# Optimization experiments

Measured on AMD Instinct MI355X. Metric: run time of the kernel, lower is better.

## Reference

```python
import jax, jax.numpy as jnp
import numpy as np
import math

SIZE = 112
GROUPS = 64

def _dct_filter(size):
    # get_dct_filter: W[i, j] = a_i * cos(pi * i / size * (j + 0.5)), a_0 = sqrt(1/size), else sqrt(2/size)
    i = np.arange(size)[:, None].astype(np.float64)
    j = np.arange(size)[None, :].astype(np.float64)
    a = np.where(i == 0, math.sqrt(1.0 / size), math.sqrt(2.0 / size))
    return (a * np.cos(np.pi * i / size * (j + 0.5))).astype(np.float32)

def _band_mask(size, groups):
    # Faithful to the source: d = sqrt((xx ^ 2) + (yy ^ 2)) where ^ is PYTHON BITWISE XOR (a bug in the
    # original, reproduced here). Keep entry if i*mul <= d < (i+1)*mul, else overwrite with 1e-8.
    mul = size // 8
    xs = np.bitwise_xor(np.arange(size), 2).astype(np.float64)
    d = np.sqrt(xs[:, None] + xs[None, :])            # [size, size], indexed [xx, yy]
    i = np.arange(groups).astype(np.float64)[:, None, None]
    keep = (d[None, :, :] >= i * mul) & (d[None, :, :] < (i + 1) * mul)  # [groups, size, size]
    return keep

_MASK = jnp.asarray(_band_mask(SIZE, GROUPS))

def setup_inputs() -> dict:
    key = jax.random.key(0)
    x = jax.random.normal(key, (64, GROUPS, SIZE, SIZE), dtype=jnp.float32)
    W = jnp.asarray(_dct_filter(SIZE))  # module's DCT-II basis buffer
    return {"x": x, "W": W}

def reference(x, W):
    # 2D DCT-II over spatial dims expressed as two matmuls with the module's own DCT filter:
    # Y[b,c] = W @ X[b,c] @ W^T   (fused replacement for the CPU round-trip dct(x))
    y = jnp.einsum('ik,bckl,jl->bcij', W, x, W)
    # Static radial-band mask per frequency group; outside-band entries are set to 1e-8.
    return jnp.where(_MASK[None], y, jnp.float32(1e-8))
```

## Files before the change

### kernel.cpp

```cpp
#include <hip/hip_runtime.h>


#define SIZE  112
#define TILE  (SIZE * SIZE)
#define TILE4 (TILE / 4)
#define NCOMPUTE 512
#define FILLV 1e-8f

#define DOT4(a, b) ((a).x*(b).x + (a).y*(b).y + (a).z*(b).z + (a).w*(b).w)

__global__ __launch_bounds__(256)
void dct_band_kernel(const float* __restrict__ x,
                     const float* __restrict__ W,
                     float* __restrict__ out)
{
    const int tid = threadIdx.x;
    const int blk = blockIdx.x;

    if (blk >= NCOMPUTE) {
        const int f = blk - NCOMPUTE;
        const int b = f / 62;
        const int c = 2 + f % 62;
        float4* o4 = (float4*)(out + (size_t)(b * 64 + c) * TILE);
        const float4 v = make_float4(FILLV, FILLV, FILLV, FILLV);
        #pragma unroll
        for (int n = 0; n < 13; ++n) {
            int e = tid + n * 256;
            if (e < TILE4) o4[e] = v;
        }
        return;
    }

    __shared__ float4 regA[3248];
    __shared__ float4 Usm[784];

    const int q  = blk & 3;
    const int t  = blk >> 2;
    const int b  = t >> 1;
    const int c  = t & 1;
    const int i0 = 28 * q;
    const size_t tOff = (size_t)(b * 64 + c) * TILE;

    const float4* x4 = (const float4*)(x + tOff);
    #pragma unroll
    for (int n = 0; n < 13; ++n) {
        int e = tid + n * 256;
        if (e < TILE4) regA[e] = x4[e];
    }
    __syncthreads();

    if (tid < 196) {
        const int diq = tid / 28;
        const int l4  = tid % 28;
        float4 u0 = make_float4(0,0,0,0), u1 = u0, u2 = u0, u3 = u0;
        const float* wr0 = W + (i0 + 4 * diq) * SIZE;
        const float* wr1 = wr0 + SIZE;
        const float* wr2 = wr1 + SIZE;
        const float* wr3 = wr2 + SIZE;
        #pragma unroll 4
        for (int k = 0; k < SIZE; ++k) {
            float4 xv = regA[k * 28 + l4];
            float w0 = wr0[k], w1 = wr1[k], w2 = wr2[k], w3 = wr3[k];
            u0.x += w0 * xv.x; u0.y += w0 * xv.y; u0.z += w0 * xv.z; u0.w += w0 * xv.w;
            u1.x += w1 * xv.x; u1.y += w1 * xv.y; u1.z += w1 * xv.z; u1.w += w1 * xv.w;
            u2.x += w2 * xv.x; u2.y += w2 * xv.y; u2.z += w2 * xv.z; u2.w += w2 * xv.w;
            u3.x += w3 * xv.x; u3.y += w3 * xv.y; u3.z += w3 * xv.z; u3.w += w3 * xv.w;
        }
        const int ub = 4 * diq * 28 + l4;
        Usm[ub]          = u0;
        Usm[ub + 28]     = u1;
        Usm[ub + 56]     = u2;
        Usm[ub + 84]     = u3;
    }
    __syncthreads();

    const float4* W4 = (const float4*)W;
    #pragma unroll
    for (int n = 0; n < 13; ++n) {
        int e = tid + n * 256;
        if (e < TILE4) {
            int j = e / 28;
            int p = e % 28;
            regA[(j >> 2) * 113 + (j & 3) * 28 + p] = W4[e];
        }
    }
    __syncthreads();

    if (tid < 196) {
        const int dq = tid / 28;
        const int jq = tid % 28;
        float acc[4][4];
        #pragma unroll
        for (int a = 0; a < 4; ++a)
            #pragma unroll
            for (int d = 0; d < 4; ++d) acc[a][d] = 0.f;

        const float4* Ur = Usm + 4 * dq * 28;
        const float4* Wb = regA + jq * 113;
        #pragma unroll 2
        for (int l = 0; l < 28; ++l) {
            float4 u0 = Ur[l], u1 = Ur[l + 28], u2 = Ur[l + 56], u3 = Ur[l + 84];
            float4 w0 = Wb[l], w1 = Wb[l + 28], w2 = Wb[l + 56], w3 = Wb[l + 84];
            acc[0][0] += DOT4(u0, w0); acc[0][1] += DOT4(u0, w1);
            acc[0][2] += DOT4(u0, w2); acc[0][3] += DOT4(u0, w3);
            acc[1][0] += DOT4(u1, w0); acc[1][1] += DOT4(u1, w1);
            acc[1][2] += DOT4(u1, w2); acc[1][3] += DOT4(u1, w3);
            acc[2][0] += DOT4(u2, w0); acc[2][1] += DOT4(u2, w1);
            acc[2][2] += DOT4(u2, w2); acc[2][3] += DOT4(u2, w3);
            acc[3][0] += DOT4(u3, w0); acc[3][1] += DOT4(u3, w1);
            acc[3][2] += DOT4(u3, w2); acc[3][3] += DOT4(u3, w3);
        }

        const int j0 = 4 * jq;
        const bool g1 = (c != 0);
        #pragma unroll
        for (int mi = 0; mi < 4; ++mi) {
            const int i  = i0 + 4 * dq + mi;
            const int xi = i ^ 2;
            float4 res;
            res.x = (((xi + ((j0 + 0) ^ 2)) < 196) != g1) ? acc[mi][0] : FILLV;
            res.y = (((xi + ((j0 + 1) ^ 2)) < 196) != g1) ? acc[mi][1] : FILLV;
            res.z = (((xi + ((j0 + 2) ^ 2)) < 196) != g1) ? acc[mi][2] : FILLV;
            res.w = (((xi + ((j0 + 3) ^ 2)) < 196) != g1) ? acc[mi][3] : FILLV;
            ((float4*)(out + tOff + (size_t)i * SIZE))[jq] = res;
        }
    }
}

extern "C" void kernel_launch(void* const* d_in, const int* in_sizes, int n_in,
                              void* d_out, int out_size, void* d_ws, size_t ws_size,
                              hipStream_t stream) {
    const float* x = (const float*)d_in[0];
    const float* W = (const float*)d_in[1];
    float* out = (float*)d_out;
    (void)in_sizes; (void)n_in; (void)out_size; (void)d_ws; (void)ws_size;
    dct_band_kernel<<<dim3(NCOMPUTE + 64 * 62), dim3(256), 0, stream>>>(x, W, out);
}
```

Baseline: 315.2 us.

## Stream x in k-chunks, read W from global, nontemporal fill stores

The first matmul now stages x in four 28-row chunks with a small shared buffer instead of loading the whole 112x112 tile, cutting shared memory from about 64KB to about 25KB so more blocks can be resident. The second stage reads W rows directly from global/L2 instead of staging a padded transposed copy in LDS. The fill-only blocks use nontemporal stores for the constant 1e-8 output. The trade-offs are extra barriers per chunk and uncached-in-LDS global W reads in the inner loop.

```diff
diff --git a/kernel.cpp b/kernel.cpp
--- a/kernel.cpp
+++ b/kernel.cpp
@@ -4,8 +4,11 @@
 #define SIZE  112
 #define TILE  (SIZE * SIZE)
 #define TILE4 (TILE / 4)
+#define ROW4  (SIZE / 4)
 #define NCOMPUTE 512
 #define FILLV 1e-8f
+
+typedef float floatx4 __attribute__((ext_vector_type(4)));
 
 #define DOT4(a, b) ((a).x*(b).x + (a).y*(b).y + (a).z*(b).z + (a).w*(b).w)
 
@@ -21,17 +24,17 @@
         const int f = blk - NCOMPUTE;
         const int b = f / 62;
         const int c = 2 + f % 62;
-        float4* o4 = (float4*)(out + (size_t)(b * 64 + c) * TILE);
-        const float4 v = make_float4(FILLV, FILLV, FILLV, FILLV);
+        floatx4* o4 = (floatx4*)(out + (size_t)(b * 64 + c) * TILE);
+        const floatx4 v = {FILLV, FILLV, FILLV, FILLV};
         #pragma unroll
         for (int n = 0; n < 13; ++n) {
             int e = tid + n * 256;
-            if (e < TILE4) o4[e] = v;
+            if (e < TILE4) __builtin_nontemporal_store(v, o4 + e);
         }
         return;
     }
 
-    __shared__ float4 regA[3248];
+    __shared__ float4 Xs[784];
     __shared__ float4 Usm[784];
 
     const int q  = blk & 3;
@@ -40,49 +43,44 @@
     const int c  = t & 1;
     const int i0 = 28 * q;
     const size_t tOff = (size_t)(b * 64 + c) * TILE;
+    const float4* x4 = (const float4*)(x + tOff);
 
-    const float4* x4 = (const float4*)(x + tOff);
-    #pragma unroll
-    for (int n = 0; n < 13; ++n) {
-        int e = tid + n * 256;
-        if (e < TILE4) regA[e] = x4[e];
+    const int diq = tid / 28;
+    const int l4  = tid % 28;
+    float4 u0 = make_float4(0,0,0,0), u1 = u0, u2 = u0, u3 = u0;
+
+    for (int kp = 0; kp < 4; ++kp) {
+        #pragma unroll
+        for (int n = 0; n < 4; ++n) {
+            int e = tid + n * 256;
+            if (e < 784) Xs[e] = x4[kp * 784 + e];
+        }
+        __syncthreads();
+
+        if (tid < 196) {
+            const float* wr0 = W + (i0 + 4 * diq) * SIZE + kp * 28;
+            const float* wr1 = wr0 + SIZE;
+            const float* wr2 = wr1 + SIZE;
+            const float* wr3 = wr2 + SIZE;
+            #pragma unroll 4
+            for (int k = 0; k < 28; ++k) {
+                float4 xv = Xs[k * 28 + l4];
+                float w0 = wr0[k], w1 = wr1[k], w2 = wr2[k], w3 = wr3[k];
+                u0.x += w0 * xv.x; u0.y += w0 * xv.y; u0.z += w0 * xv.z; u0.w += w0 * xv.w;
+                u1.x += w1 * xv.x; u1.y += w1 * xv.y; u1.z += w1 * xv.z; u1.w += w1 * xv.w;
+                u2.x += w2 * xv.x; u2.y += w2 * xv.y; u2.z += w2 * xv.z; u2.w += w2 * xv.w;
+                u3.x += w3 * xv.x; u3.y += w3 * xv.y; u3.z += w3 * xv.z; u3.w += w3 * xv.w;
+            }
+        }
+        __syncthreads();
     }
-    __syncthreads();
 
     if (tid < 196) {
-        const int diq = tid / 28;
-        const int l4  = tid % 28;
-        float4 u0 = make_float4(0,0,0,0), u1 = u0, u2 = u0, u3 = u0;
-        const float* wr0 = W + (i0 + 4 * diq) * SIZE;
-        const float* wr1 = wr0 + SIZE;
-        const float* wr2 = wr1 + SIZE;
-        const float* wr3 = wr2 + SIZE;
-        #pragma unroll 4
-        for (int k = 0; k < SIZE; ++k) {
-            float4 xv = regA[k * 28 + l4];
-            float w0 = wr0[k], w1 = wr1[k], w2 = wr2[k], w3 = wr3[k];
-            u0.x += w0 * xv.x; u0.y += w0 * xv.y; u0.z += w0 * xv.z; u0.w += w0 * xv.w;
-            u1.x += w1 * xv.x; u1.y += w1 * xv.y; u1.z += w1 * xv.z; u1.w += w1 * xv.w;
-            u2.x += w2 * xv.x; u2.y += w2 * xv.y; u2.z += w2 * xv.z; u2.w += w2 * xv.w;
-            u3.x += w3 * xv.x; u3.y += w3 * xv.y; u3.z += w3 * xv.z; u3.w += w3 * xv.w;
-        }
         const int ub = 4 * diq * 28 + l4;
-        Usm[ub]          = u0;
-        Usm[ub + 28]     = u1;
-        Usm[ub + 56]     = u2;
-        Usm[ub + 84]     = u3;
-    }
-    __syncthreads();
-
-    const float4* W4 = (const float4*)W;
-    #pragma unroll
-    for (int n = 0; n < 13; ++n) {
-        int e = tid + n * 256;
-        if (e < TILE4) {
-            int j = e / 28;
-            int p = e % 28;
-            regA[(j >> 2) * 113 + (j & 3) * 28 + p] = W4[e];
-        }
+        Usm[ub]      = u0;
+        Usm[ub + 28] = u1;
+        Usm[ub + 56] = u2;
+        Usm[ub + 84] = u3;
     }
     __syncthreads();
 
@@ -96,19 +94,23 @@
             for (int d = 0; d < 4; ++d) acc[a][d] = 0.f;
 
         const float4* Ur = Usm + 4 * dq * 28;
-        const float4* Wb = regA + jq * 113;
+        const float4* W4 = (const float4*)W;
+        const float4* w0 = W4 + (4 * jq + 0) * ROW4;
+        const float4* w1 = W4 + (4 * jq + 1) * ROW4;
+        const float4* w2 = W4 + (4 * jq + 2) * ROW4;
+        const float4* w3 = W4 + (4 * jq + 3) * ROW4;
         #pragma unroll 2
         for (int l = 0; l < 28; ++l) {
-            float4 u0 = Ur[l], u1 = Ur[l + 28], u2 = Ur[l + 56], u3 = Ur[l + 84];
-            float4 w0 = Wb[l], w1 = Wb[l + 28], w2 = Wb[l + 56], w3 = Wb[l + 84];
-            acc[0][0] += DOT4(u0, w0); acc[0][1] += DOT4(u0, w1);
-            acc[0][2] += DOT4(u0, w2); acc[0][3] += DOT4(u0, w3);
-            acc[1][0] += DOT4(u1, w0); acc[1][1] += DOT4(u1, w1);
-            acc[1][2] += DOT4(u1, w2); acc[1][3] += DOT4(u1, w3);
-            acc[2][0] += DOT4(u2, w0); acc[2][1] += DOT4(u2, w1);
-            acc[2][2] += DOT4(u2, w2); acc[2][3] += DOT4(u2, w3);
-            acc[3][0] += DOT4(u3, w0); acc[3][1] += DOT4(u3, w1);
-            acc[3][2] += DOT4(u3, w2); acc[3][3] += DOT4(u3, w3);
+            float4 uv0 = Ur[l], uv1 = Ur[l + 28], uv2 = Ur[l + 56], uv3 = Ur[l + 84];
+            float4 wv0 = w0[l], wv1 = w1[l], wv2 = w2[l], wv3 = w3[l];
+            acc[0][0] += DOT4(uv0, wv0); acc[0][1] += DOT4(uv0, wv1);
+            acc[0][2] += DOT4(uv0, wv2); acc[0][3] += DOT4(uv0, wv3);
+            acc[1][0] += DOT4(uv1, wv0); acc[1][1] += DOT4(uv1, wv1);
+            acc[1][2] += DOT4(uv1, wv2); acc[1][3] += DOT4(uv1, wv3);
+            acc[2][0] += DOT4(uv2, wv0); acc[2][1] += DOT4(uv2, wv1);
+            acc[2][2] += DOT4(uv2, wv2); acc[2][3] += DOT4(uv2, wv3);
+            acc[3][0] += DOT4(uv3, wv0); acc[3][1] += DOT4(uv3, wv1);
+            acc[3][2] += DOT4(uv3, wv2); acc[3][3] += DOT4(uv3, wv3);
         }
 
         const int j0 = 4 * jq;
```

New measurement: 323.1 us. +2.5%, slower.
